# Optimization experiments

Hardware: AMD Instinct MI355X
Metric: run time of the kernel (lower is better)

The kernel has to match this reference:

```python
import jax, jax.numpy as jnp
import numpy as np

GAMMA = 0.5
TEMP = 0.1
EPS_NORM = 1e-12  # torch F.normalize eps


def setup_inputs() -> dict:
    key = jax.random.key(0)
    k1, k2, k3, k4, k5 = jax.random.split(key, 5)
    B, D = 2048, 1024
    S, H = 128, 512
    latents = jax.random.normal(k1, (B, D), dtype=jnp.float32)
    reconstructed = jax.random.normal(k2, (B, S, H), dtype=jnp.float32)
    target = jax.random.normal(k3, (B, S, H), dtype=jnp.float32)
    mask = jax.random.uniform(k4, (B, S), dtype=jnp.float32)
    behavior_labels = jax.random.randint(k5, (B,), 0, 16, dtype=jnp.int32)
    return {"latents": latents, "reconstructed": reconstructed, "target": target,
            "mask": mask, "behavior_labels": behavior_labels}


def _supcon_loss(latents, behavior_labels):
    B = latents.shape[0]
    # cosine similarity matrix [B, B] / temperature
    n = latents / jnp.clip(jnp.linalg.norm(latents, axis=-1, keepdims=True), EPS_NORM)
    sim = jnp.matmul(n, n.T) / TEMP
    eye = jnp.eye(B, dtype=bool)
    pos = (behavior_labels[:, None] == behavior_labels[None, :]) & (~eye)
    # denom per anchor: sum over j != i of exp(sim[i, j])  (stable via logsumexp)
    log_denom = jax.scipy.special.logsumexp(jnp.where(eye, -jnp.inf, sim), axis=1)
    num_pos = pos.sum(axis=1)
    mean_pos_sim = jnp.where(pos, sim, 0.0).sum(axis=1) / jnp.maximum(num_pos, 1).astype(sim.dtype)
    # per-anchor loss: -mean_p log(exp(sim[i,p]) / denom) = log_denom - mean_pos_sim
    loss_i = log_denom - mean_pos_sim
    valid = num_pos > 0
    num_valid = jnp.maximum(valid.sum(), 1).astype(sim.dtype)
    return jnp.where(valid, loss_i, 0.0).sum() / num_valid


def _recon_loss_mse(predicted, target, mask):
    token_error = jnp.mean((predicted - target) ** 2, axis=-1)  # [B, S]
    return (token_error * mask).sum() / jnp.maximum(mask.sum(), 1.0)


def reference(latents, reconstructed, target, mask, behavior_labels):
    loss_contrast = _supcon_loss(latents, behavior_labels)
    loss_recon = _recon_loss_mse(reconstructed, target, mask)
    total = GAMMA * loss_contrast + (1.0 - GAMMA) * loss_recon
    return total, loss_contrast, loss_recon
```

## Files before the change

kernel.cpp:

```cpp
#include <hip/hip_runtime.h>
#include <math.h>


#define TEMP_INV 10.0f
#define GAMMA 0.5f

using short8 = __attribute__((ext_vector_type(8))) short;
using f32x4  = __attribute__((ext_vector_type(4))) float;

__device__ __forceinline__ float blockReduceSum(float v) {
    __shared__ float red[8];
    #pragma unroll
    for (int off = 32; off > 0; off >>= 1) v += __shfl_down(v, off, 64);
    int lane = threadIdx.x & 63, wid = threadIdx.x >> 6;
    __syncthreads();
    if (lane == 0) red[wid] = v;
    __syncthreads();
    float r = 0.f;
    if (threadIdx.x == 0) {
        int nw = (blockDim.x + 63) >> 6;
        for (int w = 0; w < nw; ++w) r += red[w];
    }
    return r;
}

__device__ __forceinline__ unsigned short f2bf(float f) {
    unsigned u = __float_as_uint(f);
    unsigned r = (u + 0x7FFFu + ((u >> 16) & 1u)) >> 16;
    return (unsigned short)r;
}

__global__ void norm_convert_kernel(const float* __restrict__ x,
                                    unsigned short* __restrict__ nbf, int D) {
    int row = blockIdx.x;
    const float4* xr = (const float4*)(x + (size_t)row * D);
    unsigned short* nr = nbf + (size_t)row * D;
    int n4 = D >> 2;
    float s = 0.f;
    for (int i = threadIdx.x; i < n4; i += blockDim.x) {
        float4 v = xr[i];
        s += v.x * v.x + v.y * v.y + v.z * v.z + v.w * v.w;
    }
    float tot = blockReduceSum(s);
    __shared__ float s_inv;
    if (threadIdx.x == 0) s_inv = 1.0f / fmaxf(sqrtf(tot), 1e-12f);
    __syncthreads();
    float inv = s_inv;
    for (int i = threadIdx.x; i < n4; i += blockDim.x) {
        float4 v = xr[i];
        ushort4 o;
        o.x = f2bf(v.x * inv); o.y = f2bf(v.y * inv);
        o.z = f2bf(v.z * inv); o.w = f2bf(v.w * inv);
        *(ushort4*)(nr + i * 4) = o;
    }
}

__launch_bounds__(256)
__global__ void fused_kernel(const short* __restrict__ nbf,
                             const int* __restrict__ labels,
                             const f32x4* __restrict__ p4,
                             const f32x4* __restrict__ t4,
                             const float* __restrict__ mask,
                             float* __restrict__ denomAcc,
                             float* __restrict__ posAcc,
                             float* __restrict__ cntAcc,
                             float* __restrict__ racc,
                             float* __restrict__ msum,
                             int B, int D,
                             unsigned n4, int shiftH4, unsigned nBS4,
                             int nbx, int NC, int NR) {
    constexpr int BM = 128, BK = 64;
    __shared__ short lds[2 * BM * BK];
    short* As = lds;
    short* Bs = lds + BM * BK;

    const int tid = threadIdx.x;
    const int role = blockIdx.x;

    if (role < NC) {
        const int lane = tid & 63;
        const int w    = tid >> 6;
        const int wr   = w >> 1, wc = w & 1;
        const int brow = (role / nbx) * BM;
        const int bcol = (role % nbx) * BM;
        const int g    = lane >> 4, l15 = lane & 15;

        f32x4 acc[4][4] = {};

        for (int k0 = 0; k0 < D; k0 += BK) {
            #pragma unroll
            for (int i = 0; i < 4; ++i) {
                int chunk = i * 256 + tid;
                int r  = chunk >> 3;
                int cu = chunk & 7;
                int su = cu ^ (r & 7);
                uint4 va = *(const uint4*)(nbf + (size_t)(brow + r) * D + k0 + cu * 8);
                *(uint4*)(As + r * BK + su * 8) = va;
                uint4 vb = *(const uint4*)(nbf + (size_t)(bcol + r) * D + k0 + cu * 8);
                *(uint4*)(Bs + r * BK + su * 8) = vb;
            }
            __syncthreads();

            short8 a[4][2], b[4][2];
            #pragma unroll
            for (int mi = 0; mi < 4; ++mi) {
                int ra = wr * 64 + mi * 16 + l15;
                int rb = wc * 64 + mi * 16 + l15;
                #pragma unroll
                for (int ks = 0; ks < 2; ++ks) {
                    int ua = (ks * 4 + g) ^ (ra & 7);
                    a[mi][ks] = *(const short8*)(As + ra * BK + ua * 8);
                    int ub = (ks * 4 + g) ^ (rb & 7);
                    b[mi][ks] = *(const short8*)(Bs + rb * BK + ub * 8);
                }
            }
            #pragma unroll
            for (int ks = 0; ks < 2; ++ks)
                #pragma unroll
                for (int mi = 0; mi < 4; ++mi)
                    #pragma unroll
                    for (int ni = 0; ni < 4; ++ni)
                        acc[mi][ni] = __builtin_amdgcn_mfma_f32_16x16x32_bf16(
                            a[mi][ks], b[ni][ks], acc[mi][ni], 0, 0, 0);
            __syncthreads();
        }

        int lc[4], gcv[4];
        #pragma unroll
        for (int ni = 0; ni < 4; ++ni) {
            gcv[ni] = bcol + wc * 64 + ni * 16 + l15;
            lc[ni]  = labels[gcv[ni]];
        }
        #pragma unroll
        for (int mi = 0; mi < 4; ++mi) {
            #pragma unroll
            for (int r = 0; r < 4; ++r) {
                int R  = brow + wr * 64 + mi * 16 + g * 4 + r;
                int lr = labels[R];
                float d = 0.f, p = 0.f, c = 0.f;
                #pragma unroll
                for (int ni = 0; ni < 4; ++ni) {
                    float sim = acc[mi][ni][r] * TEMP_INV;
                    if (R != gcv[ni]) {
                        d += __expf(sim - TEMP_INV);
                        if (lr == lc[ni]) { p += sim; c += 1.f; }
                    }
                }
                #pragma unroll
                for (int off = 8; off > 0; off >>= 1) {
                    d += __shfl_down(d, off, 16);
                    p += __shfl_down(p, off, 16);
                    c += __shfl_down(c, off, 16);
                }
                if (l15 == 0) {
                    atomicAdd(&denomAcc[R], d);
                    atomicAdd(&posAcc[R], p);
                    atomicAdd(&cntAcc[R], c);
                }
            }
        }
    } else if (role < NC + NR) {
        unsigned i = (unsigned)(role - NC) * blockDim.x + tid;
        unsigned stride = (unsigned)NR * blockDim.x;
        float local = 0.f;
        for (; i < n4; i += stride) {
            f32x4 a = __builtin_nontemporal_load(&p4[i]);
            f32x4 b = __builtin_nontemporal_load(&t4[i]);
            float m = mask[i >> shiftH4];
            f32x4 dfl = a - b;
            local += m * (dfl[0] * dfl[0] + dfl[1] * dfl[1] +
                          dfl[2] * dfl[2] + dfl[3] * dfl[3]);
        }
        float tot = blockReduceSum(local);
        if (tid == 0) atomicAdd(racc, tot);
    } else {
        int nm = gridDim.x - NC - NR;
        unsigned i = (unsigned)(role - NC - NR) * blockDim.x + tid;
        unsigned stride = (unsigned)nm * blockDim.x;
        float local = 0.f;
        for (; i < nBS4; i += stride) {
            f32x4 m = *(const f32x4*)(mask + 4 * (size_t)i);
            local += m[0] + m[1] + m[2] + m[3];
        }
        float tot = blockReduceSum(local);
        if (tid == 0) atomicAdd(msum, tot);
    }
}

__global__ void finalize_kernel(const float* __restrict__ denom, const float* __restrict__ pos,
                                const float* __restrict__ cnt, const float* __restrict__ racc,
                                const float* __restrict__ msum, float* __restrict__ out,
                                int B, float invH) {
    float lsum = 0.f, vcnt = 0.f;
    for (int r = threadIdx.x; r < B; r += blockDim.x) {
        float c = cnt[r];
        if (c > 0.5f) {
            float ld = logf(denom[r]) + TEMP_INV;
            lsum += ld - pos[r] / c;
            vcnt += 1.f;
        }
    }
    lsum = blockReduceSum(lsum);
    vcnt = blockReduceSum(vcnt);
    if (threadIdx.x == 0) {
        float contrast = lsum / fmaxf(vcnt, 1.f);
        float recon = racc[0] * invH / fmaxf(msum[0], 1.f);
        out[0] = GAMMA * contrast + (1.f - GAMMA) * recon;
        out[1] = contrast;
        out[2] = recon;
    }
}

extern "C" void kernel_launch(void* const* d_in, const int* in_sizes, int n_in,
                              void* d_out, int out_size, void* d_ws, size_t ws_size,
                              hipStream_t stream) {
    const float* latents = (const float*)d_in[0];
    const float* recon   = (const float*)d_in[1];
    const float* target  = (const float*)d_in[2];
    const float* mask    = (const float*)d_in[3];
    const int*   labels  = (const int*)d_in[4];
    float* out = (float*)d_out;
    float* ws  = (float*)d_ws;

    int B = in_sizes[4];
    int D = in_sizes[0] / B;
    int S = in_sizes[3] / B;
    int H = (in_sizes[1] / B) / S;

    float* denom = ws;
    float* pos   = ws + B;
    float* cnt   = ws + 2 * B;
    float* racc  = ws + 3 * B;
    float* msum  = ws + 3 * B + 1;
    unsigned short* nbf = (unsigned short*)(ws + 3 * B + 64);

    hipMemsetAsync(d_ws, 0, (size_t)(3 * B + 64) * sizeof(float), stream);

    norm_convert_kernel<<<B, 256, 0, stream>>>(latents, nbf, D);

    int nbx = B / 128;
    int NC = nbx * nbx;
    int NR = 1536;
    int NM = 16;
    unsigned n4 = (unsigned)B * (unsigned)S * (unsigned)(H / 4);
    unsigned nBS4 = (unsigned)(B * S) / 4;
    int shiftH4 = __builtin_ctz((unsigned)(H / 4));

    fused_kernel<<<NC + NR + NM, 256, 0, stream>>>(
        (const short*)nbf, labels, (const f32x4*)recon, (const f32x4*)target,
        mask, denom, pos, cnt, racc, msum,
        B, D, n4, shiftH4, nBS4, nbx, NC, NR);

    finalize_kernel<<<1, 256, 0, stream>>>(denom, pos, cnt, racc, msum, out, B, 1.0f / H);
}
```

Measured before the change: 228.2 us.

## Fold finalize into fused kernel via last-block counter and tune occupancy

Drops the separate finalize launch by having each block increment a done counter, with the last block computing the final losses from the atomic accumulators. It also adds a min-blocks hint of 4 to launch bounds and restructures the MFMA loop so fragments are loaded per k-step, which lowers register pressure. The recon stream loop is unrolled by two to keep more loads in flight. The cost is an extra global atomic and fence per block, and the last block runs the serial finalize work.

```diff
diff --git a/kernel.cpp b/kernel.cpp
--- a/kernel.cpp
+++ b/kernel.cpp
@@ -55,7 +55,7 @@
     }
 }
 
-__launch_bounds__(256)
+__launch_bounds__(256, 4)
 __global__ void fused_kernel(const short* __restrict__ nbf,
                              const int* __restrict__ labels,
                              const f32x4* __restrict__ p4,
@@ -66,7 +66,9 @@
                              float* __restrict__ cntAcc,
                              float* __restrict__ racc,
                              float* __restrict__ msum,
-                             int B, int D,
+                             unsigned* __restrict__ doneCnt,
+                             float* __restrict__ out,
+                             int B, int D, float invH,
                              unsigned n4, int shiftH4, unsigned nBS4,
                              int nbx, int NC, int NR) {
     constexpr int BM = 128, BK = 64;
@@ -101,27 +103,26 @@
             }
             __syncthreads();
 
-            short8 a[4][2], b[4][2];
             #pragma unroll
-            for (int mi = 0; mi < 4; ++mi) {
-                int ra = wr * 64 + mi * 16 + l15;
-                int rb = wc * 64 + mi * 16 + l15;
-                #pragma unroll
-                for (int ks = 0; ks < 2; ++ks) {
+            for (int ks = 0; ks < 2; ++ks) {
+                short8 b[4];
+                #pragma unroll
+                for (int ni = 0; ni < 4; ++ni) {
+                    int rb = wc * 64 + ni * 16 + l15;
+                    int ub = (ks * 4 + g) ^ (rb & 7);
+                    b[ni] = *(const short8*)(Bs + rb * BK + ub * 8);
+                }
+                #pragma unroll
+                for (int mi = 0; mi < 4; ++mi) {
+                    int ra = wr * 64 + mi * 16 + l15;
                     int ua = (ks * 4 + g) ^ (ra & 7);
-                    a[mi][ks] = *(const short8*)(As + ra * BK + ua * 8);
-                    int ub = (ks * 4 + g) ^ (rb & 7);
-                    b[mi][ks] = *(const short8*)(Bs + rb * BK + ub * 8);
-                }
-            }
-            #pragma unroll
-            for (int ks = 0; ks < 2; ++ks)
-                #pragma unroll
-                for (int mi = 0; mi < 4; ++mi)
+                    short8 a = *(const short8*)(As + ra * BK + ua * 8);
                     #pragma unroll
                     for (int ni = 0; ni < 4; ++ni)
                         acc[mi][ni] = __builtin_amdgcn_mfma_f32_16x16x32_bf16(
-                            a[mi][ks], b[ni][ks], acc[mi][ni], 0, 0, 0);
+                            a, b[ni], acc[mi][ni], 0, 0, 0);
+                }
+            }
             __syncthreads();
         }
 
@@ -160,16 +161,26 @@
             }
         }
     } else if (role < NC + NR) {
+        unsigned stride = (unsigned)NR * blockDim.x;
         unsigned i = (unsigned)(role - NC) * blockDim.x + tid;
-        unsigned stride = (unsigned)NR * blockDim.x;
         float local = 0.f;
-        for (; i < n4; i += stride) {
-            f32x4 a = __builtin_nontemporal_load(&p4[i]);
-            f32x4 b = __builtin_nontemporal_load(&t4[i]);
-            float m = mask[i >> shiftH4];
-            f32x4 dfl = a - b;
-            local += m * (dfl[0] * dfl[0] + dfl[1] * dfl[1] +
-                          dfl[2] * dfl[2] + dfl[3] * dfl[3]);
+        for (; i + stride < n4; i += 2 * stride) {
+            f32x4 a0 = __builtin_nontemporal_load(&p4[i]);
+            f32x4 b0 = __builtin_nontemporal_load(&t4[i]);
+            f32x4 a1 = __builtin_nontemporal_load(&p4[i + stride]);
+            f32x4 b1 = __builtin_nontemporal_load(&t4[i + stride]);
+            float m0 = mask[i >> shiftH4];
+            float m1 = mask[(i + stride) >> shiftH4];
+            f32x4 d0 = a0 - b0, d1 = a1 - b1;
+            local += m0 * (d0[0]*d0[0] + d0[1]*d0[1] + d0[2]*d0[2] + d0[3]*d0[3]);
+            local += m1 * (d1[0]*d1[0] + d1[1]*d1[1] + d1[2]*d1[2] + d1[3]*d1[3]);
+        }
+        if (i < n4) {
+            f32x4 a0 = __builtin_nontemporal_load(&p4[i]);
+            f32x4 b0 = __builtin_nontemporal_load(&t4[i]);
+            float m0 = mask[i >> shiftH4];
+            f32x4 d0 = a0 - b0;
+            local += m0 * (d0[0]*d0[0] + d0[1]*d0[1] + d0[2]*d0[2] + d0[3]*d0[3]);
         }
         float tot = blockReduceSum(local);
         if (tid == 0) atomicAdd(racc, tot);
@@ -185,29 +196,37 @@
         float tot = blockReduceSum(local);
         if (tid == 0) atomicAdd(msum, tot);
     }
-}
-
-__global__ void finalize_kernel(const float* __restrict__ denom, const float* __restrict__ pos,
-                                const float* __restrict__ cnt, const float* __restrict__ racc,
-                                const float* __restrict__ msum, float* __restrict__ out,
-                                int B, float invH) {
-    float lsum = 0.f, vcnt = 0.f;
-    for (int r = threadIdx.x; r < B; r += blockDim.x) {
-        float c = cnt[r];
-        if (c > 0.5f) {
-            float ld = logf(denom[r]) + TEMP_INV;
-            lsum += ld - pos[r] / c;
-            vcnt += 1.f;
-        }
-    }
-    lsum = blockReduceSum(lsum);
-    vcnt = blockReduceSum(vcnt);
-    if (threadIdx.x == 0) {
-        float contrast = lsum / fmaxf(vcnt, 1.f);
-        float recon = racc[0] * invH / fmaxf(msum[0], 1.f);
-        out[0] = GAMMA * contrast + (1.f - GAMMA) * recon;
-        out[1] = contrast;
-        out[2] = recon;
+
+    __shared__ unsigned s_old;
+    __syncthreads();
+    if (tid == 0) {
+        __threadfence();
+        s_old = atomicAdd(doneCnt, 1u);
+    }
+    __syncthreads();
+    if (s_old == gridDim.x - 1) {
+        __threadfence();
+        float lsum = 0.f, vcnt = 0.f;
+        for (int r = tid; r < B; r += blockDim.x) {
+            float c = __hip_atomic_load(&cntAcc[r], __ATOMIC_RELAXED, __HIP_MEMORY_SCOPE_AGENT);
+            if (c > 0.5f) {
+                float dn = __hip_atomic_load(&denomAcc[r], __ATOMIC_RELAXED, __HIP_MEMORY_SCOPE_AGENT);
+                float ps = __hip_atomic_load(&posAcc[r], __ATOMIC_RELAXED, __HIP_MEMORY_SCOPE_AGENT);
+                lsum += (logf(dn) + TEMP_INV) - ps / c;
+                vcnt += 1.f;
+            }
+        }
+        lsum = blockReduceSum(lsum);
+        vcnt = blockReduceSum(vcnt);
+        if (tid == 0) {
+            float ra = __hip_atomic_load(racc, __ATOMIC_RELAXED, __HIP_MEMORY_SCOPE_AGENT);
+            float ms = __hip_atomic_load(msum, __ATOMIC_RELAXED, __HIP_MEMORY_SCOPE_AGENT);
+            float contrast = lsum / fmaxf(vcnt, 1.f);
+            float recon = ra * invH / fmaxf(ms, 1.f);
+            out[0] = GAMMA * contrast + (1.f - GAMMA) * recon;
+            out[1] = contrast;
+            out[2] = recon;
+        }
     }
 }
 
@@ -232,6 +251,7 @@
     float* cnt   = ws + 2 * B;
     float* racc  = ws + 3 * B;
     float* msum  = ws + 3 * B + 1;
+    unsigned* doneCnt = (unsigned*)(ws + 3 * B + 2);
     unsigned short* nbf = (unsigned short*)(ws + 3 * B + 64);
 
     hipMemsetAsync(d_ws, 0, (size_t)(3 * B + 64) * sizeof(float), stream);
@@ -248,8 +268,6 @@
 
     fused_kernel<<<NC + NR + NM, 256, 0, stream>>>(
         (const short*)nbf, labels, (const f32x4*)recon, (const f32x4*)target,
-        mask, denom, pos, cnt, racc, msum,
-        B, D, n4, shiftH4, nBS4, nbx, NC, NR);
-
-    finalize_kernel<<<1, 256, 0, stream>>>(denom, pos, cnt, racc, msum, out, B, 1.0f / H);
-}
+        mask, denom, pos, cnt, racc, msum, doneCnt, out,
+        B, D, 1.0f / H, n4, shiftH4, nBS4, nbx, NC, NR);
+}
```

Result: slower. 269.7 us (+18.2%).
